# Kernel optimization log

Hardware: AMD Instinct MI355X
Metric: run time of the kernel (lower is better)

Reference implementation:

```python
import jax, jax.numpy as jnp
import numpy as np

N_TILES, NX = 6, 96
IN_C, HID_C = 128, 256
BATCH = 4


def _build_neighbors(n_tiles=N_TILES, nx=NX):
    # 4-connectivity on each tile with periodic wrap (fixed cubed-sphere-style
    # grid graph; preserves the gather/mean access pattern of build_dgl_graph).
    i, j = np.meshgrid(np.arange(nx), np.arange(nx), indexing='ij')
    idx = lambda ii, jj: (ii % nx) * nx + (jj % nx)
    per_tile = np.stack([idx(i - 1, j), idx(i + 1, j), idx(i, j - 1), idx(i, j + 1)],
                        axis=-1).reshape(nx * nx, 4)
    offsets = (np.arange(n_tiles) * nx * nx)[:, None, None]
    return (per_tile[None] + offsets).reshape(-1, 4).astype(np.int32)


def setup_inputs() -> dict:
    key = jax.random.key(0)
    ks = jax.random.split(key, 6)
    s = lambda fan_in: 1.0 / np.sqrt(fan_in)
    return {
        'x': jax.random.normal(ks[0], (BATCH, N_TILES, NX, NX, IN_C), jnp.float32),
        'neighbors': jnp.asarray(_build_neighbors()),
        'W_self1': jax.random.normal(ks[1], (IN_C, HID_C), jnp.float32) * s(IN_C),
        'W_neigh1': jax.random.normal(ks[2], (IN_C, HID_C), jnp.float32) * s(IN_C),
        'b1': jnp.zeros((HID_C,), jnp.float32),
        'W_self2': jax.random.normal(ks[3], (HID_C, HID_C), jnp.float32) * s(HID_C),
        'W_neigh2': jax.random.normal(ks[4], (HID_C, HID_C), jnp.float32) * s(HID_C),
        'b2': jnp.zeros((HID_C,), jnp.float32),
    }


def _sage_conv(h, neighbors, W_self, W_neigh, b):
    # h: [B, N, C]; neighbors: [N, 4] -> mean-aggregated SAGEConv
    h_neigh = jnp.mean(h[:, neighbors], axis=2)  # [B, N, 4, C] -> [B, N, C]
    return jnp.einsum('bnc,cd->bnd', h, W_self) + \
           jnp.einsum('bnc,cd->bnd', h_neigh, W_neigh) + b


def reference(x, neighbors, W_self1, W_neigh1, b1, W_self2, W_neigh2, b2):
    B, T, X, Y, C = x.shape
    h = x.reshape(B, T * X * Y, C)                      # flatten sphere -> nodes
    h = jax.nn.relu(_sage_conv(h, neighbors, W_self1, W_neigh1, b1))
    h = jax.nn.relu(_sage_conv(h, neighbors, W_self2, W_neigh2, b2))
    return h.reshape(B, T, X, Y, -1)
```

## Files before the change

kernel.cpp:

```cpp
#include <hip/hip_runtime.h>
#include <stdint.h>

typedef __attribute__((ext_vector_type(8))) short short8;
typedef __attribute__((ext_vector_type(4))) float f32x4;

#define NNODES 55296
#define DOUT 256

#define WAIT_VM(N) asm volatile("s_waitcnt vmcnt(" #N ")" ::: "memory")
#define SOFT_FENCE asm volatile("" ::: "memory")

__device__ __forceinline__ float bf2f(unsigned short h) {
    union { unsigned u; float f; } x; x.u = ((unsigned)h) << 16; return x.f;
}
__device__ __forceinline__ unsigned short f2bf(float f) {
    union { float f; unsigned u; } x; x.f = f;
    return (unsigned short)((x.u + 0x7fffu + ((x.u >> 16) & 1u)) >> 16);
}

__device__ __forceinline__ void storev(float* p, float v) { *p = v; }
__device__ __forceinline__ void storev(unsigned short* p, float v) { *p = f2bf(v); }

__device__ __forceinline__ void dma16(const void* g, void* l) {
    __builtin_amdgcn_global_load_lds(
        reinterpret_cast<const unsigned int __attribute__((address_space(1)))*>((uintptr_t)g),
        reinterpret_cast<unsigned int __attribute__((address_space(3)))*>((uintptr_t)l),
        16, 0, 0);
}

__device__ __forceinline__ short8 frag_self(const float* p) {
    float4 a = *(const float4*)p, b = *(const float4*)(p + 4);
    union { short8 s; unsigned short u[8]; } r;
    r.u[0] = f2bf(a.x); r.u[1] = f2bf(a.y); r.u[2] = f2bf(a.z); r.u[3] = f2bf(a.w);
    r.u[4] = f2bf(b.x); r.u[5] = f2bf(b.y); r.u[6] = f2bf(b.z); r.u[7] = f2bf(b.w);
    return r.s;
}
__device__ __forceinline__ short8 frag_self(const unsigned short* p) {
    return *(const short8*)p;
}
__device__ __forceinline__ void acc8(const float* p, float* o) {
    float4 a = *(const float4*)p, b = *(const float4*)(p + 4);
    o[0] += a.x; o[1] += a.y; o[2] += a.z; o[3] += a.w;
    o[4] += b.x; o[5] += b.y; o[6] += b.z; o[7] += b.w;
}
__device__ __forceinline__ void acc8(const unsigned short* p, float* o) {
    uint4 v = *(const uint4*)p;
    const unsigned short* u = (const unsigned short*)&v;
#pragma unroll
    for (int i = 0; i < 8; ++i) o[i] += bf2f(u[i]);
}
template <typename TIN>
__device__ __forceinline__ short8 frag_mean4(const TIN* p0, const TIN* p1,
                                             const TIN* p2, const TIN* p3) {
    float s[8] = {0.f, 0.f, 0.f, 0.f, 0.f, 0.f, 0.f, 0.f};
    acc8(p0, s); acc8(p1, s); acc8(p2, s); acc8(p3, s);
    union { short8 s8; unsigned short u[8]; } r;
#pragma unroll
    for (int i = 0; i < 8; ++i) r.u[i] = f2bf(s[i] * 0.25f);
    return r.s8;
}

__global__ void build_wt(const float* __restrict__ Ws,
                         const float* __restrict__ Wn,
                         unsigned short* __restrict__ Wt, int C) {
    int K2 = 2 * C;
    int idx = blockIdx.x * 256 + threadIdx.x;
    if (idx >= 256 * K2) return;
    int d = idx / K2;
    int k = idx - d * K2;
    float v = (k < C) ? Ws[(size_t)k * DOUT + d] : Wn[(size_t)(k - C) * DOUT + d];
    Wt[idx] = f2bf(v);
}

__global__ void build_wt_pm(const float* __restrict__ Ws,
                            const float* __restrict__ Wn,
                            unsigned short* __restrict__ Wp, int C) {
    int K2 = 2 * C;
    int idx = blockIdx.x * 256 + threadIdx.x;
    if (idx >= 256 * K2) return;
    int d = idx / K2;
    int k = idx - d * K2;
    float v = (k < C) ? Ws[(size_t)k * DOUT + d] : Wn[(size_t)(k - C) * DOUT + d];
    int q = k >> 6;
    int kqb = (k & 63) * 2;
    int byte = q * 32768 + d * 128 + (kqb ^ ((d & 7) << 4));
    Wp[byte >> 1] = f2bf(v);
}

__global__ __launch_bounds__(256) void mean_xb_pm(const float* __restrict__ x,
                                                  const int* __restrict__ nbr,
                                                  unsigned short* __restrict__ xm,
                                                  int mTot) {
    const int idx = blockIdx.x * 256 + threadIdx.x;
    const int node = idx >> 4;
    const int ch = (idx & 15) * 8;
    const int b = node / NNODES;
    const int n = node - b * NNODES;
    const size_t bbase = (size_t)b * NNODES;
    const int4 nb = *(const int4*)(nbr + (size_t)n * 4);
    const float* ps = x + (size_t)node * 128 + ch;
    union { uint4 v; unsigned short u[8]; } rs, rm;
    float4 a0 = *(const float4*)ps, a1 = *(const float4*)(ps + 4);
    rs.u[0] = f2bf(a0.x); rs.u[1] = f2bf(a0.y); rs.u[2] = f2bf(a0.z); rs.u[3] = f2bf(a0.w);
    rs.u[4] = f2bf(a1.x); rs.u[5] = f2bf(a1.y); rs.u[6] = f2bf(a1.z); rs.u[7] = f2bf(a1.w);
    float s[8] = {0.f, 0.f, 0.f, 0.f, 0.f, 0.f, 0.f, 0.f};
    acc8(x + (bbase + nb.x) * 128 + ch, s);
    acc8(x + (bbase + nb.y) * 128 + ch, s);
    acc8(x + (bbase + nb.z) * 128 + ch, s);
    acc8(x + (bbase + nb.w) * 128 + ch, s);
#pragma unroll
    for (int i = 0; i < 8; ++i) rm.u[i] = f2bf(s[i] * 0.25f);
    const size_t cs = (size_t)mTot * 32;
    *(uint4*)(xm + (size_t)(ch >> 5) * cs + (size_t)node * 32 + (ch & 31)) = rs.v;
    *(uint4*)(xm + (size_t)(4 + (ch >> 5)) * cs + (size_t)node * 32 + (ch & 31)) = rm.v;
}

__global__ __launch_bounds__(256) void mean_pass_pm(const unsigned short* __restrict__ h1,
                                                    const int* __restrict__ nbr,
                                                    unsigned short* __restrict__ hm,
                                                    int mTot) {
    const int idx = blockIdx.x * 256 + threadIdx.x;
    const int node = idx >> 5;
    const int ch = (idx & 31) * 8;
    const int b = node / NNODES;
    const int n = node - b * NNODES;
    const size_t bbase = (size_t)b * NNODES;
    const int4 nb = *(const int4*)(nbr + (size_t)n * 4);
    const size_t cs = (size_t)mTot * 32;
    const size_t co = (size_t)(ch >> 5) * cs + (ch & 31);
    float s[8] = {0.f, 0.f, 0.f, 0.f, 0.f, 0.f, 0.f, 0.f};
    acc8(h1 + co + (bbase + nb.x) * 32, s);
    acc8(h1 + co + (bbase + nb.y) * 32, s);
    acc8(h1 + co + (bbase + nb.z) * 32, s);
    acc8(h1 + co + (bbase + nb.w) * 32, s);
    union { uint4 v; unsigned short u[8]; } r;
#pragma unroll
    for (int i = 0; i < 8; ++i) r.u[i] = f2bf(s[i] * 0.25f);
    *(uint4*)(hm + co + (size_t)node * 32) = r.v;
}

template <int NK, typename TOUT>
__global__ __launch_bounds__(256) void sage_v14(
    const unsigned short* __restrict__ a0p,
    const unsigned short* __restrict__ a1p,
    const unsigned short* __restrict__ Wp,
    const float* __restrict__ bias,
    TOUT* __restrict__ out,
    int nwg, int mTot) {
    extern __shared__ char lds[];
    const int tid = threadIdx.x;
    const int bid = blockIdx.x;
    const int wk = (bid & 7) * (nwg >> 3) + (bid >> 3);
    const int yg = wk & 1;
    const int rb = wk >> 1;
    const int gcol0 = yg * 128;
    const int rowbase = rb * 128;

    const int l = tid & 63, w = tid >> 6;
    const int lr = l & 15, lg = l >> 4;
    const int rowg = w >> 1;
    const int colb = (w & 1) * 64;

    const size_t chstride = (size_t)mTot * 64;

    auto stageW = [&](int q) {
        char* wb = lds + ((q & 1) << 14);
        const char* src = (const char*)Wp + (size_t)q * 32768 + (size_t)gcol0 * 128;
#pragma unroll
        for (int i = 0; i < 4; ++i) {
            int o = w * 4096 + i * 1024;
            dma16(src + o + l * 16, wb + o + l * 16);
        }
    };
    auto issueA = [&](int p) {
        const char* base = (NK == 16 && p >= 8) ? (const char*)a1p : (const char*)a0p;
        const char* src = base + (size_t)(p & 7) * chstride + (size_t)rowbase * 64;
        char* ring = lds + 32768 + (p & 3) * 8192;
#pragma unroll
        for (int i = 0; i < 2; ++i) {
            int o = w * 2048 + i * 1024;
            dma16(src + o + l * 16, ring + o + l * 16);
        }
    };

    stageW(0); issueA(0); issueA(1); issueA(2);

    f32x4 acc[4][4];
#pragma unroll
    for (int m = 0; m < 4; ++m)
#pragma unroll
        for (int j = 0; j < 4; ++j) acc[m][j] = (f32x4){0.f, 0.f, 0.f, 0.f};

#pragma unroll
    for (int kk = 0; kk < NK; ++kk) {
        int n;
        if (kk == 0) n = 4;
        else if (kk & 1) n = ((kk + 1 < NK) ? 6 : 0) + ((kk + 2 < NK) ? 2 : 0);
        else n = 2 + ((kk + 2 < NK) ? 2 : 0);
        switch (n) {
            case 0: WAIT_VM(0); break;
            case 2: WAIT_VM(2); break;
            case 4: WAIT_VM(4); break;
            case 6: WAIT_VM(6); break;
            default: WAIT_VM(8); break;
        }
        __builtin_amdgcn_s_barrier();
        SOFT_FENCE;

        if (((kk & 1) == 0) && (kk + 2 < NK)) stageW((kk + 2) >> 1);
        if (kk + 3 < NK) issueA(kk + 3);

        const int bufo = 32768 + (kk & 3) * 8192;
        short8 af[4];
#pragma unroll
        for (int m = 0; m < 4; ++m)
            af[m] = *(const short8*)(lds + bufo +
                                     ((rowg * 4 + m) * 16 + lr) * 64 + lg * 16);

        char* wbuf = lds + (((kk >> 1) & 1) << 14);
        const int kq0 = ((kk & 1) << 6) | (lg << 4);
#pragma unroll
        for (int j = 0; j < 4; ++j) {
            const int col = colb + j * 16 + lr;
            const short8 wf = *(const short8*)(
                wbuf + (col << 7) + (kq0 ^ ((lr & 7) << 4)));
#pragma unroll
            for (int m = 0; m < 4; ++m)
                acc[m][j] = __builtin_amdgcn_mfma_f32_16x16x32_bf16(wf, af[m], acc[m][j], 0, 0, 0);
        }
        SOFT_FENCE;
    }

#pragma unroll
    for (int m = 0; m < 4; ++m) {
        const int row = rowbase + rowg * 64 + m * 16 + lr;
#pragma unroll
        for (int j = 0; j < 4; ++j) {
            const int gcol = gcol0 + colb + j * 16 + lg * 4;
            const float4 bv = *(const float4*)(bias + gcol);
            float o0 = fmaxf(acc[m][j][0] + bv.x, 0.f);
            float o1 = fmaxf(acc[m][j][1] + bv.y, 0.f);
            float o2 = fmaxf(acc[m][j][2] + bv.z, 0.f);
            float o3 = fmaxf(acc[m][j][3] + bv.w, 0.f);
            if constexpr (sizeof(TOUT) == 4) {
                float4 o = {o0, o1, o2, o3};
                *(float4*)((float*)out + (size_t)row * 256 + gcol) = o;
            } else {
                union { unsigned short u[4]; uint2 v; } pk;
                pk.u[0] = f2bf(o0); pk.u[1] = f2bf(o1);
                pk.u[2] = f2bf(o2); pk.u[3] = f2bf(o3);
                unsigned short* hp = (unsigned short*)out +
                    (size_t)(gcol >> 5) * ((size_t)mTot * 32) +
                    (size_t)row * 32 + (gcol & 31);
                *(uint2*)hp = pk.v;
            }
        }
    }
}

template <int C, typename TIN, typename TOUT>
__global__ __launch_bounds__(512, 2) void sage_v3(
    const TIN* __restrict__ hin, const int* __restrict__ nbr,
    const unsigned short* __restrict__ Wt, const float* __restrict__ bias,
    TOUT* __restrict__ out) {
    constexpr int K2 = 2 * C;
    constexpr int ROWB = K2 * 2;
    constexpr int LCOLS = 131072 / ROWB;
    constexpr int CG = LCOLS / 128;
    constexpr int RG = 8 / CG;
    extern __shared__ char Bs[];

    const int tid = threadIdx.x;
    const int gcol0 = blockIdx.y * LCOLS;
    {
        const char* src = (const char*)(Wt + (size_t)gcol0 * K2);
#pragma unroll
        for (int i = 0; i < 16; ++i) {
            int byt = (i * 512 + tid) * 16;
            uint4 v = *(const uint4*)(src + byt);
            int c = byt / ROWB;
            *(uint4*)(Bs + (byt ^ ((c & 7) << 4))) = v;
        }
    }
    __syncthreads();

    const int l = tid & 63;
    const int w = tid >> 6;
    const int rowg = w / CG;
    const int colb = (w % CG) * 128;
    const int lr = l & 15, lg = l >> 4;

    const int rowbase = blockIdx.x * (RG * 64) + rowg * 64;
    const int bb = rowbase / NNODES;
    const int n0 = rowbase - bb * NNODES;
    const size_t bbase = (size_t)bb * NNODES;

    unsigned soff[4], noff[4][4];
#pragma unroll
    for (int m = 0; m < 4; ++m) {
        int r = m * 16 + lr;
        soff[m] = (unsigned)(((rowbase + r) * (size_t)C + lg * 8) * sizeof(TIN));
        int4 nb = *(const int4*)(nbr + (size_t)(n0 + r) * 4);
        noff[m][0] = (unsigned)(((bbase + nb.x) * C + lg * 8) * sizeof(TIN));
        noff[m][1] = (unsigned)(((bbase + nb.y) * C + lg * 8) * sizeof(TIN));
        noff[m][2] = (unsigned)(((bbase + nb.z) * C + lg * 8) * sizeof(TIN));
        noff[m][3] = (unsigned)(((bbase + nb.w) * C + lg * 8) * sizeof(TIN));
    }
    const char* hb = (const char*)hin;

    f32x4 acc[4][8];
#pragma unroll
    for (int m = 0; m < 4; ++m)
#pragma unroll
        for (int j = 0; j < 8; ++j) acc[m][j] = (f32x4){0.f, 0.f, 0.f, 0.f};

#pragma unroll
    for (int kk = 0; kk < K2 / 32; ++kk) {
        const int k0 = kk * 32;
        short8 a[4];
        if (k0 < C) {
            const unsigned kb = k0 * sizeof(TIN);
#pragma unroll
            for (int m = 0; m < 4; ++m)
                a[m] = frag_self((const TIN*)(hb + soff[m] + kb));
        } else {
            const unsigned kb = (k0 - C) * sizeof(TIN);
#pragma unroll
            for (int m = 0; m < 4; ++m)
                a[m] = frag_mean4((const TIN*)(hb + noff[m][0] + kb),
                                  (const TIN*)(hb + noff[m][1] + kb),
                                  (const TIN*)(hb + noff[m][2] + kb),
                                  (const TIN*)(hb + noff[m][3] + kb));
        }
#pragma unroll
        for (int j = 0; j < 8; ++j) {
            const int c = colb + j * 16 + lr;
            const short8 bf = *(const short8*)(
                Bs + ((c * ROWB + (k0 + lg * 8) * 2) ^ ((l & 7) << 4)));
#pragma unroll
            for (int m = 0; m < 4; ++m)
                acc[m][j] = __builtin_amdgcn_mfma_f32_16x16x32_bf16(a[m], bf, acc[m][j], 0, 0, 0);
        }
    }

#pragma unroll
    for (int j = 0; j < 8; ++j) {
        const int gcol = gcol0 + colb + j * 16 + lr;
        const float bv = bias[gcol];
#pragma unroll
        for (int m = 0; m < 4; ++m) {
#pragma unroll
            for (int r = 0; r < 4; ++r) {
                const int row = rowbase + m * 16 + lg * 4 + r;
                storev(out + (size_t)row * DOUT + gcol, fmaxf(acc[m][j][r] + bv, 0.f));
            }
        }
    }
}

extern "C" void kernel_launch(void* const* d_in, const int* in_sizes, int n_in,
                              void* d_out, int out_size, void* d_ws, size_t ws_size,
                              hipStream_t stream) {
    const float* x = (const float*)d_in[0];
    const int* nbr = (const int*)d_in[1];
    const float* Ws1 = (const float*)d_in[2];
    const float* Wn1 = (const float*)d_in[3];
    const float* b1 = (const float*)d_in[4];
    const float* Ws2 = (const float*)d_in[5];
    const float* Wn2 = (const float*)d_in[6];
    const float* b2 = (const float*)d_in[7];
    float* out = (float*)d_out;

    const int B = in_sizes[0] / (NNODES * 128);
    const int M = B * NNODES;

    char* ws = (char*)d_ws;
    const size_t h1_bytes = (size_t)M * DOUT * 2;
    const size_t hm_bytes = (size_t)M * DOUT * 2;
    const size_t need = h1_bytes + hm_bytes + 131072 + 262144;

    if (ws_size >= need) {
        unsigned short* h1 = (unsigned short*)ws;
        unsigned short* xm = (unsigned short*)(ws + h1_bytes);
        unsigned short* W1p = (unsigned short*)(ws + h1_bytes + hm_bytes);
        unsigned short* W2p = W1p + 256 * 256;

        build_wt_pm<<<256, 256, 0, stream>>>(Ws1, Wn1, W1p, 128);
        build_wt_pm<<<512, 256, 0, stream>>>(Ws2, Wn2, W2p, 256);

        hipFuncSetAttribute((const void*)sage_v14<8, unsigned short>,
                            hipFuncAttributeMaxDynamicSharedMemorySize, 65536);
        hipFuncSetAttribute((const void*)sage_v14<16, float>,
                            hipFuncAttributeMaxDynamicSharedMemorySize, 65536);

        const int nwg = (M / 128) * 2;

        mean_xb_pm<<<M / 16, 256, 0, stream>>>(x, nbr, xm, M);
        sage_v14<8, unsigned short>
            <<<nwg, 256, 65536, stream>>>(xm, xm, W1p, b1, h1, nwg, M);
        mean_pass_pm<<<M / 8, 256, 0, stream>>>(h1, nbr, xm, M);
        sage_v14<16, float>
            <<<nwg, 256, 65536, stream>>>(h1, xm, W2p, b2, out, nwg, M);
    } else {
        unsigned short* h1 = (unsigned short*)ws;
        unsigned short* Wt1 = (unsigned short*)(ws + h1_bytes);
        unsigned short* Wt2 = Wt1 + 256 * 256;

        build_wt<<<256, 256, 0, stream>>>(Ws1, Wn1, Wt1, 128);
        build_wt<<<512, 256, 0, stream>>>(Ws2, Wn2, Wt2, 256);

        hipFuncSetAttribute((const void*)sage_v3<128, float, unsigned short>,
                            hipFuncAttributeMaxDynamicSharedMemorySize, 131072);
        hipFuncSetAttribute((const void*)sage_v3<256, unsigned short, float>,
                            hipFuncAttributeMaxDynamicSharedMemorySize, 131072);

        sage_v3<128, float, unsigned short>
            <<<dim3(M / 256, 1), 512, 131072, stream>>>(x, nbr, Wt1, b1, h1);
        sage_v3<256, unsigned short, float>
            <<<dim3(M / 512, 2), 512, 131072, stream>>>(h1, nbr, Wt2, b2, out);
    }
}
```

Baseline: 320.7 us.

## Double K-step per iteration with 3-deep 16KB A ring and per-step W staging

```diff
diff --git a/kernel.cpp b/kernel.cpp
--- a/kernel.cpp
+++ b/kernel.cpp
@@ -140,7 +140,7 @@
 }
 
 template <int NK, typename TOUT>
-__global__ __launch_bounds__(256) void sage_v14(
+__global__ __launch_bounds__(256) void sage_v15(
     const unsigned short* __restrict__ a0p,
     const unsigned short* __restrict__ a1p,
     const unsigned short* __restrict__ Wp,
@@ -163,9 +163,9 @@
 
     const size_t chstride = (size_t)mTot * 64;
 
-    auto stageW = [&](int q) {
-        char* wb = lds + ((q & 1) << 14);
-        const char* src = (const char*)Wp + (size_t)q * 32768 + (size_t)gcol0 * 128;
+    auto stageW = [&](int p) {
+        char* wb = lds + ((p & 1) << 14);
+        const char* src = (const char*)Wp + (size_t)p * 32768 + (size_t)gcol0 * 128;
 #pragma unroll
         for (int i = 0; i < 4; ++i) {
             int o = w * 4096 + i * 1024;
@@ -173,17 +173,22 @@
         }
     };
     auto issueA = [&](int p) {
-        const char* base = (NK == 16 && p >= 8) ? (const char*)a1p : (const char*)a0p;
-        const char* src = base + (size_t)(p & 7) * chstride + (size_t)rowbase * 64;
-        char* ring = lds + 32768 + (p & 3) * 8192;
-#pragma unroll
-        for (int i = 0; i < 2; ++i) {
-            int o = w * 2048 + i * 1024;
-            dma16(src + o + l * 16, ring + o + l * 16);
+        const char* base = (p >= 4) ? (const char*)a1p : (const char*)a0p;
+        const char* src = base + (size_t)((2 * p) & 7) * chstride + (size_t)rowbase * 64;
+        char* ring = lds + 32768 + (p % 3) * 16384;
+#pragma unroll
+        for (int s = 0; s < 2; ++s) {
+            const char* cs_ = src + (size_t)s * chstride;
+            char* dst = ring + s * 8192;
+#pragma unroll
+            for (int i = 0; i < 2; ++i) {
+                int o = w * 2048 + i * 1024;
+                dma16(cs_ + o + l * 16, dst + o + l * 16);
+            }
         }
     };
 
-    stageW(0); issueA(0); issueA(1); issueA(2);
+    stageW(0); issueA(0); issueA(1);
 
     f32x4 acc[4][4];
 #pragma unroll
@@ -193,40 +198,32 @@
 
 #pragma unroll
     for (int kk = 0; kk < NK; ++kk) {
-        int n;
-        if (kk == 0) n = 4;
-        else if (kk & 1) n = ((kk + 1 < NK) ? 6 : 0) + ((kk + 2 < NK) ? 2 : 0);
-        else n = 2 + ((kk + 2 < NK) ? 2 : 0);
-        switch (n) {
-            case 0: WAIT_VM(0); break;
-            case 2: WAIT_VM(2); break;
-            case 4: WAIT_VM(4); break;
-            case 6: WAIT_VM(6); break;
-            default: WAIT_VM(8); break;
-        }
+        if (kk == NK - 1) { WAIT_VM(0); } else { WAIT_VM(4); }
         __builtin_amdgcn_s_barrier();
         SOFT_FENCE;
 
-        if (((kk & 1) == 0) && (kk + 2 < NK)) stageW((kk + 2) >> 1);
-        if (kk + 3 < NK) issueA(kk + 3);
-
-        const int bufo = 32768 + (kk & 3) * 8192;
-        short8 af[4];
-#pragma unroll
-        for (int m = 0; m < 4; ++m)
-            af[m] = *(const short8*)(lds + bufo +
-                                     ((rowg * 4 + m) * 16 + lr) * 64 + lg * 16);
-
-        char* wbuf = lds + (((kk >> 1) & 1) << 14);
-        const int kq0 = ((kk & 1) << 6) | (lg << 4);
-#pragma unroll
-        for (int j = 0; j < 4; ++j) {
-            const int col = colb + j * 16 + lr;
-            const short8 wf = *(const short8*)(
-                wbuf + (col << 7) + (kq0 ^ ((lr & 7) << 4)));
+        if (kk + 1 < NK) stageW(kk + 1);
+        if (kk + 2 < NK) issueA(kk + 2);
+
+        const int ringo = 32768 + (kk % 3) * 16384;
+        char* wbuf = lds + ((kk & 1) << 14);
+#pragma unroll
+        for (int sub = 0; sub < 2; ++sub) {
+            short8 af[4];
 #pragma unroll
             for (int m = 0; m < 4; ++m)
-                acc[m][j] = __builtin_amdgcn_mfma_f32_16x16x32_bf16(wf, af[m], acc[m][j], 0, 0, 0);
+                af[m] = *(const short8*)(lds + ringo + sub * 8192 +
+                                         ((rowg * 4 + m) * 16 + lr) * 64 + lg * 16);
+            const int kq0 = (sub << 6) | (lg << 4);
+#pragma unroll
+            for (int j = 0; j < 4; ++j) {
+                const int col = colb + j * 16 + lr;
+                const short8 wf = *(const short8*)(
+                    wbuf + (col << 7) + (kq0 ^ ((lr & 7) << 4)));
+#pragma unroll
+                for (int m = 0; m < 4; ++m)
+                    acc[m][j] = __builtin_amdgcn_mfma_f32_16x16x32_bf16(wf, af[m], acc[m][j], 0, 0, 0);
+            }
         }
         SOFT_FENCE;
     }
@@ -388,19 +385,19 @@
         build_wt_pm<<<256, 256, 0, stream>>>(Ws1, Wn1, W1p, 128);
         build_wt_pm<<<512, 256, 0, stream>>>(Ws2, Wn2, W2p, 256);
 
-        hipFuncSetAttribute((const void*)sage_v14<8, unsigned short>,
-                            hipFuncAttributeMaxDynamicSharedMemorySize, 65536);
-        hipFuncSetAttribute((const void*)sage_v14<16, float>,
-                            hipFuncAttributeMaxDynamicSharedMemorySize, 65536);
+        hipFuncSetAttribute((const void*)sage_v15<4, unsigned short>,
+                            hipFuncAttributeMaxDynamicSharedMemorySize, 81920);
+        hipFuncSetAttribute((const void*)sage_v15<8, float>,
+                            hipFuncAttributeMaxDynamicSharedMemorySize, 81920);
 
         const int nwg = (M / 128) * 2;
 
         mean_xb_pm<<<M / 16, 256, 0, stream>>>(x, nbr, xm, M);
-        sage_v14<8, unsigned short>
-            <<<nwg, 256, 65536, stream>>>(xm, xm, W1p, b1, h1, nwg, M);
+        sage_v15<4, unsigned short>
+            <<<nwg, 256, 81920, stream>>>(xm, xm, W1p, b1, h1, nwg, M);
         mean_pass_pm<<<M / 8, 256, 0, stream>>>(h1, nbr, xm, M);
-        sage_v14<16, float>
-            <<<nwg, 256, 65536, stream>>>(h1, xm, W2p, b2, out, nwg, M);
+        sage_v15<8, float>
+            <<<nwg, 256, 81920, stream>>>(h1, xm, W2p, b2, out, nwg, M);
     } else {
         unsigned short* h1 = (unsigned short*)ws;
         unsigned short* Wt1 = (unsigned short*)(ws + h1_bytes);
```

New measurement: 316.3 us, median of 2. About the same (-1.4%).
